# Kernel tuning notes

Measured on AMD Instinct MI355X. Metric: run time of the kernel, lower is better.

The kernel has to match this reference:

```python
import jax, jax.numpy as jnp
import numpy as np

NEG = -1e30  # log-domain 'zero' (safe stand-in for -inf)


def _ctc_loss(logits, labels, label_length, logit_length):
    """Dense-label CTC loss, blank = last class, logits [B,T,C] batch-major.

    Matches tf.nn.ctc_loss(blank_index=-1, logits_time_major=False):
    per-example negative log-likelihood via the standard forward algorithm
    on the blank-extended label sequence of length S = 2L+1.
    """
    B, T, C = logits.shape
    L = labels.shape[1]
    S = 2 * L + 1
    blank = C - 1

    logp = jax.nn.log_softmax(logits, axis=-1)           # [B,T,C]
    lp_t = jnp.moveaxis(logp, 1, 0)                      # [T,B,C]

    # Extended label: blank, l1, blank, l2, ..., blank
    y_ext = jnp.full((B, S), blank, dtype=labels.dtype).at[:, 1::2].set(labels)
    s_idx = jnp.arange(S)
    # s -> s-2 skip allowed iff current symbol is a non-blank differing from s-2
    y_m2 = jnp.pad(y_ext, ((0, 0), (2, 0)), constant_values=blank)[:, :-2]
    skip = (s_idx[None, :] >= 2) & (y_ext != blank) & (y_ext != y_m2)  # [B,S]

    emit0 = jnp.take_along_axis(lp_t[0], y_ext, axis=1)  # [B,S]
    alpha0 = jnp.where(s_idx[None, :] <= 1, emit0, NEG)  # paths start at s=0 or 1

    def step(alpha, lp):
        emit = jnp.take_along_axis(lp, y_ext, axis=1)                      # [B,S]
        a1 = jnp.pad(alpha, ((0, 0), (1, 0)), constant_values=NEG)[:, :-1]  # s-1
        a2 = jnp.pad(alpha, ((0, 0), (2, 0)), constant_values=NEG)[:, :-2]  # s-2
        a2 = jnp.where(skip, a2, NEG)
        new = jnp.logaddexp(jnp.logaddexp(alpha, a1), a2) + emit
        return new, new

    _, alphas = jax.lax.scan(step, alpha0, lp_t[1:])     # [T-1,B,S]
    alphas = jnp.concatenate([alpha0[None], alphas], axis=0)  # [T,B,S]

    b = jnp.arange(B)
    final = alphas[logit_length - 1, b]                  # [B,S] alpha at last frame
    end = 2 * label_length                               # index of final blank
    nll = -jnp.logaddexp(final[b, end], final[b, end - 1])
    return jnp.mean(nll)


def setup_inputs() -> dict:
    key = jax.random.key(0)
    k1, k2, k3 = jax.random.split(key, 3)
    B, T, C, L = 256, 256, 512, 64
    logits = jax.random.normal(k1, (B, T, C), dtype=jnp.float32)
    labels = jax.random.randint(k2, (B, L), 0, C - 1, dtype=jnp.int32)  # never blank
    label_length = jax.random.randint(k3, (B,), 16, L + 1, dtype=jnp.int32)
    logit_length = jnp.full((B,), T, dtype=jnp.int32)
    return {"logits": logits, "labels": labels,
            "label_length": label_length, "logit_length": logit_length}


def reference(logits, labels, label_length, logit_length):
    return _ctc_loss(logits, labels, label_length, logit_length)
```

## Files before the change

### kernel.cpp

```cpp
#include <hip/hip_runtime.h>
#include <math.h>

#define NEGV -1e30f

constexpr int Bc = 256;
constexpr int Tc = 256;
constexpr int Cc = 512;
constexpr int Lc = 64;
constexpr int NG = Tc / 4;
constexpr int NGP = NG + 2;
constexpr float INVLN2 = 1.44269504088896340736f;
constexpr float LN2    = 0.69314718055994530942f;

__device__ __forceinline__ float la2(float a, float b) {
    float m = fmaxf(a, b);
    float d = fabsf(a - b);
    return m + __log2f(exp2f(-d) + 1.0f);
}

__device__ __forceinline__ float dpp_shr1(float x, float fill) {
    int r = __builtin_amdgcn_update_dpp(__float_as_int(fill), __float_as_int(x),
                                        0x138 , 0xF, 0xF, false);
    return __int_as_float(r);
}

__global__ __launch_bounds__(256) void emit_k(const float* __restrict__ logits,
                                              const int* __restrict__ labels,
                                              float* __restrict__ lbuf,
                                              float* __restrict__ bbuf) {
    const int blk  = blockIdx.x;
    const int b    = blk >> 6;
    const int g    = blk & 63;
    const int w    = threadIdx.x >> 6;
    const int t    = g * 4 + w;
    const int lane = threadIdx.x & 63;

    __shared__ float rows[4][Cc];

    const float4* r4 = (const float4*)(logits + ((size_t)b * Tc + t) * Cc);
    float4 x0 = r4[lane];
    float4 x1 = r4[lane + 64];
    ((float4*)rows[w])[lane]      = x0;
    ((float4*)rows[w])[lane + 64] = x1;

    float e = __expf(x0.x) + __expf(x0.y) + __expf(x0.z) + __expf(x0.w)
            + __expf(x1.x) + __expf(x1.y) + __expf(x1.z) + __expf(x1.w);
#pragma unroll
    for (int o = 32; o; o >>= 1) e += __shfl_xor(e, o, 64);
    float lse2 = __log2f(e);

    int   y  = labels[b * Lc + lane];
    float xl = rows[w][y];

    lbuf[(((size_t)b * NG + g) * 64 + lane) * 4 + w] = xl * INVLN2 - lse2;
    if (lane == 63)
        bbuf[((size_t)b * NG + g) * 4 + w] = x1.w * INVLN2 - lse2;
}

__global__ __launch_bounds__(256, 4) void alpha_k(const float* __restrict__ lbuf,
                                                  const float* __restrict__ bbuf,
                                                  const int* __restrict__ labels,
                                                  const int* __restrict__ lab_len,
                                                  const int* __restrict__ log_len,
                                                  float* __restrict__ nll) {
    const int b   = blockIdx.x;
    const int tid = threadIdx.x;

    __shared__ float4 Ls[NGP * 64];
    __shared__ float4 Bs[NGP];

    {
        const float4* src = (const float4*)(lbuf + (size_t)b * NG * 64 * 4);
#pragma unroll 4
        for (int i = 0; i < 16; ++i)
            Ls[tid + i * 256] = src[tid + i * 256];
        if (tid < NG)
            Bs[tid] = ((const float4*)(bbuf + (size_t)b * NG * 4))[tid];
        if (tid >= 128 && tid < 256) {
            int j = tid - 128;
            Ls[NG * 64 + j] = make_float4(0.f, 0.f, 0.f, 0.f);
        }
        if (tid < 2) Bs[NG + tid] = make_float4(0.f, 0.f, 0.f, 0.f);
    }
    __syncthreads();
    if (tid >= 64) return;

    const int l = tid;
    const int  mylab   = labels[b * Lc + l];
    const int  prevlab = __shfl_up(mylab, 1, 64);
    const bool skip    = (l >= 1) && (mylab != prevlab);
    const int  llm1    = log_len[b] - 1;

    float ae, ao, ax;
    float fe = NEGV, fo = NEGV, fx = NEGV;

    auto step = [&](float em_l, float em_b, int t) {
        float q  = la2(ao, ae);
        float x2 = la2(ax, ao);
        float po = dpp_shr1(ao, NEGV);
        float nae = la2(ae, po) + em_b;
        float nao = (skip ? la2(q, po) : q) + em_l;
        float nax = x2 + em_b;
        ae = nae; ao = nao; ax = nax;
        if (t == llm1) { fe = ae; fo = ao; fx = ax; }
    };

    float4 lc  = Ls[l],        bc  = Bs[0];
    float4 lnx = Ls[64 + l],   bnx = Bs[1];
    float4 ln2 = Ls[128 + l],  bn2 = Bs[2];

    ae = (l == 0) ? bc.x : NEGV;
    ao = (l == 0) ? lc.x : NEGV;
    ax = NEGV;
    if (llm1 == 0) { fe = ae; fo = ao; fx = ax; }
    step(lc.y, bc.y, 1);
    step(lc.z, bc.z, 2);
    step(lc.w, bc.w, 3);

    for (int g = 1; g < NG; ++g) {
        float4 el4 = lnx, eb4 = bnx;
        lnx = ln2; bnx = bn2;
        ln2 = Ls[(g + 2) * 64 + l];
        bn2 = Bs[g + 2];
        const int t0 = g * 4;
        step(el4.x, eb4.x, t0);
        step(el4.y, eb4.y, t0 + 1);
        step(el4.z, eb4.z, t0 + 2);
        step(el4.w, eb4.w, t0 + 3);
    }

    const int L  = lab_len[b];
    float f0 = (L == 64) ? __shfl(fx, 63, 64) : __shfl(fe, L, 64);
    float f1 = __shfl(fo, L - 1, 64);
    float res = -LN2 * la2(f0, f1);
    if (l == 0) nll[b] = res;
}

__global__ __launch_bounds__(256) void reduce_k(const float* __restrict__ nll,
                                                float* __restrict__ out) {
    int tid = threadIdx.x;
    float v = nll[tid];
#pragma unroll
    for (int o = 32; o; o >>= 1) v += __shfl_xor(v, o, 64);
    __shared__ float pr[4];
    if ((tid & 63) == 0) pr[tid >> 6] = v;
    __syncthreads();
    if (tid == 0) out[0] = (pr[0] + pr[1] + pr[2] + pr[3]) * (1.0f / Bc);
}

extern "C" void kernel_launch(void* const* d_in, const int* in_sizes, int n_in,
                              void* d_out, int out_size, void* d_ws, size_t ws_size,
                              hipStream_t stream) {
    const float* logits  = (const float*)d_in[0];
    const int*   labels  = (const int*)d_in[1];
    const int*   lab_len = (const int*)d_in[2];
    const int*   log_len = (const int*)d_in[3];
    float* out  = (float*)d_out;
    float* nll  = (float*)d_ws;
    float* lbuf = (float*)((char*)d_ws + 1024);
    float* bbuf = (float*)((char*)d_ws + 1024 + (size_t)Bc * NG * 64 * 4 * 4);

    hipLaunchKernelGGL(emit_k, dim3(Bc * NG), dim3(256), 0, stream,
                       logits, labels, lbuf, bbuf);
    hipLaunchKernelGGL(alpha_k, dim3(Bc), dim3(256), 0, stream,
                       lbuf, bbuf, labels, lab_len, log_len, nll);
    hipLaunchKernelGGL(reduce_k, dim3(1), dim3(256), 0, stream, nll, out);
}
```

Baseline: 233.1 us.

## Fuse emission computation into alpha recursion with double-buffered producer-consumer waves

Merges the emission kernel and the alpha-recursion kernel into one per-batch block. Warps 1-3 (and warp 0) load logit rows and compute log-softmax emissions into double-buffered shared memory while warp 0 runs the serial recursion on the previous group. This removes the intermediate global emission buffer round-trip and a kernel launch. The cost is that only 256 blocks now stream all 128 MB of logits, so memory bandwidth may be underused, and there is a block-wide barrier every 8 timesteps.

```diff
diff --git a/kernel.cpp b/kernel.cpp
--- a/kernel.cpp
+++ b/kernel.cpp
@@ -7,8 +7,8 @@
 constexpr int Tc = 256;
 constexpr int Cc = 512;
 constexpr int Lc = 64;
-constexpr int NG = Tc / 4;
-constexpr int NGP = NG + 2;
+constexpr int GR = 8;
+constexpr int NGRP = Tc / GR;
 constexpr float INVLN2 = 1.44269504088896340736f;
 constexpr float LN2    = 0.69314718055994530942f;
 
@@ -24,116 +24,112 @@
     return __int_as_float(r);
 }
 
-__global__ __launch_bounds__(256) void emit_k(const float* __restrict__ logits,
-                                              const int* __restrict__ labels,
-                                              float* __restrict__ lbuf,
-                                              float* __restrict__ bbuf) {
-    const int blk  = blockIdx.x;
-    const int b    = blk >> 6;
-    const int g    = blk & 63;
-    const int w    = threadIdx.x >> 6;
-    const int t    = g * 4 + w;
-    const int lane = threadIdx.x & 63;
+__global__ __launch_bounds__(256) void ctc_k(const float* __restrict__ logits,
+                                             const int* __restrict__ labels,
+                                             const int* __restrict__ lab_len,
+                                             const int* __restrict__ log_len,
+                                             float* __restrict__ nll) {
+    const int b    = blockIdx.x;
+    const int tid  = threadIdx.x;
+    const int w    = tid >> 6;
+    const int lane = tid & 63;
 
-    __shared__ float rows[4][Cc];
+    __shared__ float rows[2][GR][Cc];
+    __shared__ float em_l[2][GR][64];
+    __shared__ float em_b[2][GR];
 
-    const float4* r4 = (const float4*)(logits + ((size_t)b * Tc + t) * Cc);
-    float4 x0 = r4[lane];
-    float4 x1 = r4[lane + 64];
-    ((float4*)rows[w])[lane]      = x0;
-    ((float4*)rows[w])[lane + 64] = x1;
+    const float* base = logits + (size_t)b * Tc * Cc;
+    const int y = labels[b * Lc + lane];
 
-    float e = __expf(x0.x) + __expf(x0.y) + __expf(x0.z) + __expf(x0.w)
-            + __expf(x1.x) + __expf(x1.y) + __expf(x1.z) + __expf(x1.w);
-#pragma unroll
-    for (int o = 32; o; o >>= 1) e += __shfl_xor(e, o, 64);
-    float lse2 = __log2f(e);
-
-    int   y  = labels[b * Lc + lane];
-    float xl = rows[w][y];
-
-    lbuf[(((size_t)b * NG + g) * 64 + lane) * 4 + w] = xl * INVLN2 - lse2;
-    if (lane == 63)
-        bbuf[((size_t)b * NG + g) * 4 + w] = x1.w * INVLN2 - lse2;
-}
-
-__global__ __launch_bounds__(256, 4) void alpha_k(const float* __restrict__ lbuf,
-                                                  const float* __restrict__ bbuf,
-                                                  const int* __restrict__ labels,
-                                                  const int* __restrict__ lab_len,
-                                                  const int* __restrict__ log_len,
-                                                  float* __restrict__ nll) {
-    const int b   = blockIdx.x;
-    const int tid = threadIdx.x;
-
-    __shared__ float4 Ls[NGP * 64];
-    __shared__ float4 Bs[NGP];
-
-    {
-        const float4* src = (const float4*)(lbuf + (size_t)b * NG * 64 * 4);
-#pragma unroll 4
-        for (int i = 0; i < 16; ++i)
-            Ls[tid + i * 256] = src[tid + i * 256];
-        if (tid < NG)
-            Bs[tid] = ((const float4*)(bbuf + (size_t)b * NG * 4))[tid];
-        if (tid >= 128 && tid < 256) {
-            int j = tid - 128;
-            Ls[NG * 64 + j] = make_float4(0.f, 0.f, 0.f, 0.f);
-        }
-        if (tid < 2) Bs[NG + tid] = make_float4(0.f, 0.f, 0.f, 0.f);
-    }
-    __syncthreads();
-    if (tid >= 64) return;
-
-    const int l = tid;
-    const int  mylab   = labels[b * Lc + l];
-    const int  prevlab = __shfl_up(mylab, 1, 64);
-    const bool skip    = (l >= 1) && (mylab != prevlab);
+    const int  prevlab = __shfl_up(y, 1, 64);
+    const bool skip    = (lane >= 1) && (y != prevlab);
     const int  llm1    = log_len[b] - 1;
-
-    float ae, ao, ax;
+    float ae = NEGV, ao = NEGV, ax = NEGV;
     float fe = NEGV, fo = NEGV, fx = NEGV;
 
-    auto step = [&](float em_l, float em_b, int t) {
+    auto step = [&](float em_lv, float em_bv, int t) {
         float q  = la2(ao, ae);
         float x2 = la2(ax, ao);
         float po = dpp_shr1(ao, NEGV);
-        float nae = la2(ae, po) + em_b;
-        float nao = (skip ? la2(q, po) : q) + em_l;
-        float nax = x2 + em_b;
+        float nae = la2(ae, po) + em_bv;
+        float nao = (skip ? la2(q, po) : q) + em_lv;
+        float nax = x2 + em_bv;
         ae = nae; ao = nao; ax = nax;
         if (t == llm1) { fe = ae; fo = ao; fx = ax; }
     };
 
-    float4 lc  = Ls[l],        bc  = Bs[0];
-    float4 lnx = Ls[64 + l],   bnx = Bs[1];
-    float4 ln2 = Ls[128 + l],  bn2 = Bs[2];
+    float4 A0, A1, A2, A3;
+    float4 B0, B1, B2, B3;
 
-    ae = (l == 0) ? bc.x : NEGV;
-    ao = (l == 0) ? lc.x : NEGV;
-    ax = NEGV;
-    if (llm1 == 0) { fe = ae; fo = ao; fx = ax; }
-    step(lc.y, bc.y, 1);
-    step(lc.z, bc.z, 2);
-    step(lc.w, bc.w, 3);
+    auto issue = [&](int g, float4& r0a, float4& r0b, float4& r1a, float4& r1b) {
+        const float4* p0 = (const float4*)(base + (size_t)(g * GR + w) * Cc);
+        const float4* p1 = (const float4*)(base + (size_t)(g * GR + w + 4) * Cc);
+        r0a = p0[lane]; r0b = p0[lane + 64];
+        r1a = p1[lane]; r1b = p1[lane + 64];
+    };
 
-    for (int g = 1; g < NG; ++g) {
-        float4 el4 = lnx, eb4 = bnx;
-        lnx = ln2; bnx = bn2;
-        ln2 = Ls[(g + 2) * 64 + l];
-        bn2 = Bs[g + 2];
-        const int t0 = g * 4;
-        step(el4.x, eb4.x, t0);
-        step(el4.y, eb4.y, t0 + 1);
-        step(el4.z, eb4.z, t0 + 2);
-        step(el4.w, eb4.w, t0 + 3);
+    auto row_em = [&](int s, int r, const float4& x0, const float4& x1) {
+        ((float4*)rows[s][r])[lane]      = x0;
+        ((float4*)rows[s][r])[lane + 64] = x1;
+        float e = __expf(x0.x) + __expf(x0.y) + __expf(x0.z) + __expf(x0.w)
+                + __expf(x1.x) + __expf(x1.y) + __expf(x1.z) + __expf(x1.w);
+#pragma unroll
+        for (int o = 32; o; o >>= 1) e += __shfl_xor(e, o, 64);
+        float lse2 = __log2f(e);
+        float xl = rows[s][r][y];
+        em_l[s][r][lane] = xl * INVLN2 - lse2;
+        if (lane == 63)
+            em_b[s][r] = x1.w * INVLN2 - lse2;
+    };
+
+    auto finish = [&](int s, const float4& r0a, const float4& r0b,
+                             const float4& r1a, const float4& r1b) {
+        row_em(s, w,     r0a, r0b);
+        row_em(s, w + 4, r1a, r1b);
+    };
+
+    auto consume = [&](int i, int s) {
+        const int t0 = i * GR;
+        if (i == 0) {
+            float eb = em_b[0][0];
+            float el = em_l[0][0][lane];
+            ae = (lane == 0) ? eb : NEGV;
+            ao = (lane == 0) ? el : NEGV;
+            ax = NEGV;
+            if (llm1 == 0) { fe = ae; fo = ao; fx = ax; }
+#pragma unroll
+            for (int r = 1; r < GR; ++r)
+                step(em_l[0][r][lane], em_b[0][r], r);
+        } else {
+#pragma unroll
+            for (int r = 0; r < GR; ++r)
+                step(em_l[s][r][lane], em_b[s][r], t0 + r);
+        }
+    };
+
+    issue(0, A0, A1, A2, A3);
+    issue(1, B0, B1, B2, B3);
+    finish(0, A0, A1, A2, A3);
+    __syncthreads();
+
+    for (int i = 0; i < NGRP; i += 2) {
+        if (i + 2 < NGRP) issue(i + 2, A0, A1, A2, A3);
+        finish(1, B0, B1, B2, B3);
+        if (w == 0) consume(i, 0);
+        __syncthreads();
+
+        if (i + 3 < NGRP) issue(i + 3, B0, B1, B2, B3);
+        if (i + 2 < NGRP) finish(0, A0, A1, A2, A3);
+        if (w == 0) consume(i + 1, 1);
+        __syncthreads();
     }
 
-    const int L  = lab_len[b];
-    float f0 = (L == 64) ? __shfl(fx, 63, 64) : __shfl(fe, L, 64);
-    float f1 = __shfl(fo, L - 1, 64);
-    float res = -LN2 * la2(f0, f1);
-    if (l == 0) nll[b] = res;
+    if (w == 0) {
+        const int L  = lab_len[b];
+        float f0 = (L == Lc) ? __shfl(fx, 63, 64) : __shfl(fe, L, 64);
+        float f1 = __shfl(fo, L - 1, 64);
+        if (lane == 0) nll[b] = -LN2 * la2(f0, f1);
+    }
 }
 
 __global__ __launch_bounds__(256) void reduce_k(const float* __restrict__ nll,
@@ -155,14 +151,10 @@
     const int*   labels  = (const int*)d_in[1];
     const int*   lab_len = (const int*)d_in[2];
     const int*   log_len = (const int*)d_in[3];
-    float* out  = (float*)d_out;
-    float* nll  = (float*)d_ws;
-    float* lbuf = (float*)((char*)d_ws + 1024);
-    float* bbuf = (float*)((char*)d_ws + 1024 + (size_t)Bc * NG * 64 * 4 * 4);
+    float* out = (float*)d_out;
+    float* nll = (float*)d_ws;
 
-    hipLaunchKernelGGL(emit_k, dim3(Bc * NG), dim3(256), 0, stream,
-                       logits, labels, lbuf, bbuf);
-    hipLaunchKernelGGL(alpha_k, dim3(Bc), dim3(256), 0, stream,
-                       lbuf, bbuf, labels, lab_len, log_len, nll);
+    hipLaunchKernelGGL(ctc_k, dim3(Bc), dim3(256), 0, stream,
+                       logits, labels, lab_len, log_len, nll);
     hipLaunchKernelGGL(reduce_k, dim3(1), dim3(256), 0, stream, nll, out);
 }
```

Result: faster. 222.9 us (-4.4%).
